# Kernel tuning notes

Measured on AMD Instinct MI355X. Metric: run time of the kernel, lower is better.

The kernel has to match this reference:

```python
import jax, jax.numpy as jnp
import numpy as np

B, D = 65536, 784          # batch, input features
H = 256                     # delegator feature (hidden) dim
L = 64                      # num_leaves (experts)
C = 10                      # num_classes


def setup_inputs() -> dict:
    key = jax.random.key(0)
    ks = jax.random.split(key, 7)
    s_in = 1.0 / np.sqrt(D)
    s_h = 1.0 / np.sqrt(H)
    return {
        "x": jax.random.normal(ks[0], (B, D), dtype=jnp.float32),
        "Wf": jax.random.normal(ks[1], (D, H), dtype=jnp.float32) * s_in,   # Node feature proj
        "bf": jnp.zeros((H,), dtype=jnp.float32),
        "Wr": jax.random.normal(ks[2], (D, L), dtype=jnp.float32) * s_in,   # Node router proj
        "br": jnp.zeros((L,), dtype=jnp.float32),
        "Wl": jax.random.normal(ks[3], (L, H, C), dtype=jnp.float32) * s_h,  # per-leaf linear
        "bl": jnp.zeros((L, C), dtype=jnp.float32),
    }


def reference(x, Wf, bf, Wr, br, Wl, bl):
    # Delegator (Node): features + routing probabilities
    features = jax.nn.relu(x @ Wf + bf)                 # [B, H]
    probs = jax.nn.softmax(x @ Wr + br, axis=1)         # [B, L]
    choices = jnp.argmax(probs, axis=1)                 # [B] top-1 leaf per sample
    # Per-sample leaf dispatch: gather each sample's leaf weights, then a
    # batched vec-mat product (memory-bound gather, low FLOP/byte).
    Wc = Wl[choices]                                    # [B, H, C]
    bc = bl[choices]                                    # [B, C]
    predictions = jnp.einsum("bh,bhc->bc", features, Wc) + bc  # [B, C]
    return predictions
```

## Files before the change

### kernel.cpp

```cpp
#include <hip/hip_runtime.h>
#include <stdint.h>

#define B_ROWS 65536
#define D_IN   784
#define H_DIM  256
#define L_LEAF 64
#define C_CLS  10
#define NSTEP2 25
#define BTILE2 20480
#define GAP_THRESH 0.03f

using f32x4    = __attribute__((ext_vector_type(4))) float;
using bf16x8   = __attribute__((ext_vector_type(8))) short;
using ushort8v = __attribute__((ext_vector_type(8))) unsigned short;
using ushort4v = __attribute__((ext_vector_type(4))) unsigned short;

#define O_FLAGCNT  0
#define O_CHOICES  4096
#define O_FLAGROWS (O_CHOICES + B_ROWS * 4)
#define O_WT       (O_FLAGROWS + B_ROWS * 4)
#define O_FEAT     (O_WT + NSTEP2 * BTILE2)
#define O_WLB      (O_FEAT + (size_t)B_ROWS * H_DIM * 2)
#define WLB_BYTES  ((size_t)L_LEAF * H_DIM * C_CLS * 2)
#define WS_BASE    O_WLB
#define WS_WLB     (O_WLB + WLB_BYTES)

__device__ __forceinline__ unsigned short f2bf(float f) {
    union { float f; unsigned int u; } c; c.f = f;
    unsigned int u = c.u;
    return (unsigned short)((u + 0x7fffu + ((u >> 16) & 1u)) >> 16);
}
__device__ __forceinline__ float bf2f(unsigned short u) {
    union { unsigned int u; float f; } c; c.u = ((unsigned int)u) << 16;
    return c.f;
}
__device__ __forceinline__ unsigned int cvtpk(float a, float b) {
    unsigned int r;
    asm("v_cvt_pk_bf16_f32 %0, %1, %2" : "=v"(r) : "v"(a), "v"(b));
    return r;
}
__device__ __forceinline__ void gload_lds16(const void* g, void* l) {
    __builtin_amdgcn_global_load_lds(
        (const __attribute__((address_space(1))) unsigned int*)g,
        (__attribute__((address_space(3))) unsigned int*)l, 16, 0, 0);
}

__global__ void k0_prep32(const float* __restrict__ Wf, const float* __restrict__ Wr,
                          unsigned short* __restrict__ Wt, unsigned int* __restrict__ flagcnt) {
    if (blockIdx.x == 0 && threadIdx.x == 0) *flagcnt = 0u;
    int id = blockIdx.x * 256 + threadIdx.x;
    int ts = id / 1280;
    int r  = id % 1280;
    int n  = r % 320;
    int c  = r / 320;
    int dst = ts * BTILE2 + ((n * 64 + c * 16) ^ ((n & 7) << 4));
    int ks  = ts * 32 + c * 8;
    unsigned short v[8];
    #pragma unroll
    for (int j = 0; j < 8; ++j) {
        int k = ks + j;
        float f = 0.f;
        if (k < D_IN)
            f = (n < H_DIM) ? Wf[(size_t)k * H_DIM + n]
                            : Wr[(size_t)k * L_LEAF + (n - H_DIM)];
        v[j] = f2bf(f);
    }
    *(ushort8v*)((char*)Wt + dst) = *(ushort8v*)v;
}

__global__ void k0b_wl(const float* __restrict__ Wl, unsigned short* __restrict__ Wlb) {
    int i = (blockIdx.x * 256 + threadIdx.x) * 4;
    f32x4 v = *(const f32x4*)(Wl + i);
    ushort4v h; h.x = f2bf(v.x); h.y = f2bf(v.y); h.z = f2bf(v.z); h.w = f2bf(v.w);
    *(ushort4v*)(Wlb + i) = h;
}

#define BUFB 36864
__global__ __launch_bounds__(512, 1) void k1_pipe(
    const float* __restrict__ x, const unsigned short* __restrict__ Wt,
    const float* __restrict__ bfv, const float* __restrict__ brv,
    unsigned short* __restrict__ feat, int* __restrict__ choices,
    unsigned int* __restrict__ flagcnt, int* __restrict__ flagrows)
{
    __shared__ __align__(16) char L[3 * BUFB];

    const int t  = threadIdx.x;
    const int w  = t >> 6, l = t & 63, q = l >> 4, ic = l & 15;
    const int wm = w >> 2, wn = w & 3;
    const int bm0 = blockIdx.x * 128;
    const int ntb = wn * 5;

    f32x4 acc[4][5];
    #pragma unroll
    for (int a = 0; a < 4; ++a)
        #pragma unroll
        for (int b = 0; b < 5; ++b)
            acc[a][b] = (f32x4){0.f, 0.f, 0.f, 0.f};

    const int e7  = ic & 7;
    const int pA0 = ((2 * q)     ^ e7) << 4;
    const int pA1 = ((2 * q + 1) ^ e7) << 4;
    const int rbB = (ic * 64 + (q << 4)) ^ (e7 << 4);

#define STAGE(TS, LB)                                                          \
    {                                                                          \
        const int ts_ = (TS);                                                  \
        char* Lb_ = (LB);                                                      \
        _Pragma("unroll")                                                      \
        for (int h = 0; h < 2; ++h) {                                          \
            int i_ = h * 512 + t;                                              \
            int r_ = i_ >> 3, p_ = i_ & 7;                                     \
            int c8_ = p_ ^ (r_ & 7);                                           \
            int k_ = ts_ * 32 + c8_ * 4;                                       \
            int ko_ = (k_ + 4 <= D_IN) ? k_ : 0;                               \
            gload_lds16(x + (size_t)(bm0 + r_) * D_IN + ko_, Lb_ + i_ * 16);   \
        }                                                                      \
        const char* bs_ = (const char*)Wt + (size_t)ts_ * BTILE2;              \
        char* bd_ = Lb_ + 16384;                                               \
        gload_lds16(bs_ + t * 16,          bd_ + t * 16);                      \
        gload_lds16(bs_ + (512 + t) * 16,  bd_ + (512 + t) * 16);              \
        if (t < 256)                                                           \
            gload_lds16(bs_ + (1024 + t) * 16, bd_ + (1024 + t) * 16);         \
    }

    STAGE(0, L);
    STAGE(1, L + BUFB);

    for (int ts = 0; ts < NSTEP2; ++ts) {
        if (ts < NSTEP2 - 1)
            asm volatile("s_waitcnt vmcnt(4)\ns_barrier" ::: "memory");
        else
            asm volatile("s_waitcnt vmcnt(0)\ns_barrier" ::: "memory");

        if (ts + 2 < NSTEP2) {
            char* nb = L + ((ts + 2) % 3) * BUFB;
            STAGE(ts + 2, nb);
        }

        const char* Lc = L + (ts % 3) * BUFB;
        bf16x8 af[4];
        #pragma unroll
        for (int mt = 0; mt < 4; ++mt) {
            const char* rowp = Lc + (wm * 64 + mt * 16 + ic) * 128;
            f32x4 lo = *(const f32x4*)(rowp + pA0);
            f32x4 hi = *(const f32x4*)(rowp + pA1);
            union { unsigned int u[4]; bf16x8 v; } pk;
            pk.u[0] = cvtpk(lo.x, lo.y);
            pk.u[1] = cvtpk(lo.z, lo.w);
            pk.u[2] = cvtpk(hi.x, hi.y);
            pk.u[3] = cvtpk(hi.z, hi.w);
            af[mt] = pk.v;
        }
        const char* Bb = Lc + 16384;
        __builtin_amdgcn_s_setprio(1);
        #pragma unroll
        for (int j = 0; j < 5; ++j) {
            bf16x8 b = *(const bf16x8*)(Bb + (ntb + j) * 1024 + rbB);
            #pragma unroll
            for (int mt = 0; mt < 4; ++mt)
                acc[mt][j] = __builtin_amdgcn_mfma_f32_16x16x32_bf16(af[mt], b, acc[mt][j], 0, 0, 0);
        }
        __builtin_amdgcn_s_setprio(0);
    }
#undef STAGE

    #pragma unroll
    for (int j = 0; j < 5; ++j) {
        int col = (ntb + j) * 16 + ic;
        if (col < H_DIM) {
            float bias = bfv[col];
            #pragma unroll
            for (int mt = 0; mt < 4; ++mt) {
                #pragma unroll
                for (int i = 0; i < 4; ++i) {
                    int row = bm0 + wm * 64 + mt * 16 + q * 4 + i;
                    float v = acc[mt][j][i] + bias;
                    v = v > 0.f ? v : 0.f;
                    feat[(size_t)row * H_DIM + col] = f2bf(v);
                }
            }
        }
    }
    if (wn == 3) {
        #pragma unroll
        for (int mt = 0; mt < 4; ++mt) {
            #pragma unroll
            for (int i = 0; i < 4; ++i) {
                float m1 = -1e30f, m2 = -1e30f;
                int a1 = 0;
                #pragma unroll
                for (int j = 1; j < 5; ++j) {
                    int leaf = (j - 1) * 16 + ic;
                    float v = acc[mt][j][i] + brv[leaf];
                    if (v > m1) { m2 = m1; m1 = v; a1 = leaf; }
                    else if (v > m2) { m2 = v; }
                }
                #pragma unroll
                for (int s = 1; s < 16; s <<= 1) {
                    float om1 = __shfl_xor(m1, s, 64);
                    float om2 = __shfl_xor(m2, s, 64);
                    int   oa1 = __shfl_xor(a1, s, 64);
                    bool take = (om1 > m1) || (om1 == m1 && oa1 < a1);
                    float nm2 = take ? fmaxf(om2, m1) : fmaxf(m2, om1);
                    m1 = take ? om1 : m1;
                    a1 = take ? oa1 : a1;
                    m2 = nm2;
                }
                if (ic == 0) {
                    int row = bm0 + wm * 64 + mt * 16 + q * 4 + i;
                    choices[row] = a1;
                    if (m1 - m2 < GAP_THRESH) {
                        unsigned int idx = atomicAdd(flagcnt, 1u);
                        flagrows[idx] = row;
                    }
                }
            }
        }
    }
}

__global__ __launch_bounds__(256) void k2_exact(
    const float* __restrict__ x, const float* __restrict__ Wr,
    const float* __restrict__ brv, const unsigned int* __restrict__ flagcnt,
    const int* __restrict__ flagrows, int* __restrict__ choices)
{
    __shared__ float wl[64 * 64];
    __shared__ float xl[4][64];
    const unsigned int cnt = *flagcnt;
    const int t = threadIdx.x, w = t >> 6, l = t & 63;
    for (unsigned int base = blockIdx.x * 4u; base < cnt; base += gridDim.x * 4u) {
        unsigned int ri = base + w;
        int row = (ri < cnt) ? flagrows[ri] : 0;
        const float* xr = x + (size_t)row * D_IN;
        float s0 = 0.f, s1 = 0.f, s2 = 0.f, s3 = 0.f;
        for (int kt = 0; kt < 13; ++kt) {
            int k0 = kt * 64;
            #pragma unroll
            for (int i = 0; i < 4; ++i) {
                int flat = i * 256 + t;
                int kk = flat >> 4, lq = (flat & 15) * 4;
                int kgk = k0 + kk;
                f32x4 v = (f32x4){0.f, 0.f, 0.f, 0.f};
                if (kgk < D_IN) v = *(const f32x4*)(Wr + (size_t)kgk * L_LEAF + lq);
                *(f32x4*)&wl[kk * 64 + lq] = v;
            }
            xl[w][l] = (k0 + l < D_IN) ? xr[k0 + l] : 0.f;
            __syncthreads();
            #pragma unroll
            for (int kk = 0; kk < 64; kk += 4) {
                s0 = fmaf(xl[w][kk    ], wl[(kk    ) * 64 + l], s0);
                s1 = fmaf(xl[w][kk + 1], wl[(kk + 1) * 64 + l], s1);
                s2 = fmaf(xl[w][kk + 2], wl[(kk + 2) * 64 + l], s2);
                s3 = fmaf(xl[w][kk + 3], wl[(kk + 3) * 64 + l], s3);
            }
            __syncthreads();
        }
        float v = (s0 + s1) + (s2 + s3) + brv[l];
        int a = l;
        #pragma unroll
        for (int st = 1; st < 64; st <<= 1) {
            float ov = __shfl_xor(v, st, 64);
            int   oa = __shfl_xor(a, st, 64);
            if (ov > v || (ov == v && oa < a)) { v = ov; a = oa; }
        }
        if (l == 0 && ri < cnt) choices[row] = a;
    }
}

__global__ __launch_bounds__(256) void k3_leaf(
    const unsigned short* __restrict__ feat, const int* __restrict__ choices,
    const float* __restrict__ Wl, const unsigned short* __restrict__ Wlb,
    const float* __restrict__ blv, float* __restrict__ out)
{
    const int t = threadIdx.x, wv = t >> 6, l = t & 63, g = l >> 4, i = l & 15;
    const int row = blockIdx.x * 16 + wv * 4 + g;
    const int leaf = choices[row];

    ushort8v f0 = *(const ushort8v*)(feat + (size_t)row * H_DIM + i * 16);
    ushort8v f1 = *(const ushort8v*)(feat + (size_t)row * H_DIM + i * 16 + 8);
    float fv[16];
    #pragma unroll
    for (int j = 0; j < 8; ++j) { fv[j] = bf2f(f0[j]); fv[8 + j] = bf2f(f1[j]); }

    float acc[C_CLS];
    #pragma unroll
    for (int c = 0; c < C_CLS; ++c) acc[c] = 0.f;

    if (Wlb) {
        const unsigned short* wp = Wlb + ((size_t)leaf * H_DIM + i * 16) * C_CLS;
        ushort8v wreg[20];
        #pragma unroll
        for (int j = 0; j < 20; ++j) wreg[j] = *(const ushort8v*)(wp + j * 8);
        #pragma unroll
        for (int h = 0; h < 16; ++h) {
            #pragma unroll
            for (int c = 0; c < C_CLS; ++c) {
                int e = h * C_CLS + c;
                acc[c] = fmaf(fv[h], bf2f(wreg[e >> 3][e & 7]), acc[c]);
            }
        }
    } else {
        const float* wp = Wl + ((size_t)leaf * H_DIM + i * 16) * C_CLS;
        #pragma unroll
        for (int h = 0; h < 16; ++h) {
            #pragma unroll
            for (int c = 0; c < C_CLS; ++c)
                acc[c] = fmaf(fv[h], wp[h * C_CLS + c], acc[c]);
        }
    }
    #pragma unroll
    for (int st = 1; st < 16; st <<= 1) {
        #pragma unroll
        for (int c = 0; c < C_CLS; ++c) acc[c] += __shfl_xor(acc[c], st, 64);
    }
    if (i == 0) {
        #pragma unroll
        for (int c = 0; c < C_CLS; ++c)
            out[(size_t)row * C_CLS + c] = acc[c] + blv[leaf * C_CLS + c];
    }
}

extern "C" void kernel_launch(void* const* d_in, const int* in_sizes, int n_in,
                              void* d_out, int out_size, void* d_ws, size_t ws_size,
                              hipStream_t stream) {
    if (ws_size < WS_BASE) return;
    const bool use_bf = ws_size >= WS_WLB;

    const float* x   = (const float*)d_in[0];
    const float* Wf  = (const float*)d_in[1];
    const float* bfv = (const float*)d_in[2];
    const float* Wr  = (const float*)d_in[3];
    const float* brv = (const float*)d_in[4];
    const float* Wl  = (const float*)d_in[5];
    const float* blv = (const float*)d_in[6];
    float* out = (float*)d_out;

    char* ws = (char*)d_ws;
    unsigned int*   flagcnt  = (unsigned int*)(ws + O_FLAGCNT);
    int*            choices  = (int*)(ws + O_CHOICES);
    int*            flagrows = (int*)(ws + O_FLAGROWS);
    unsigned short* Wt       = (unsigned short*)(ws + O_WT);
    unsigned short* feat     = (unsigned short*)(ws + O_FEAT);
    unsigned short* Wlb      = use_bf ? (unsigned short*)(ws + O_WLB) : (unsigned short*)0;

    hipLaunchKernelGGL(k0_prep32, dim3(125), dim3(256), 0, stream, Wf, Wr, Wt, flagcnt);
    if (use_bf)
        hipLaunchKernelGGL(k0b_wl, dim3(160), dim3(256), 0, stream, Wl, Wlb);
    hipLaunchKernelGGL(k1_pipe, dim3(B_ROWS / 128), dim3(512), 0, stream,
                       x, Wt, bfv, brv, feat, choices, flagcnt, flagrows);
    hipLaunchKernelGGL(k2_exact, dim3(1024), dim3(256), 0, stream,
                       x, Wr, brv, flagcnt, flagrows, choices);
    hipLaunchKernelGGL(k3_leaf, dim3(B_ROWS / 16), dim3(256), 0, stream,
                       feat, choices, Wl, Wlb, blv, out);
}
```

Before: 198.9 us.

## Enlarge fused GEMM block tile to 256 rows with 2x4 warp layout

The main feature/router GEMM kernel now processes 256 rows per block instead of 128. Its eight warps are rearranged as 4x2, so each warp computes 4x10 MFMA tiles instead of 4x5. This halves how many times the weight tile is loaded per row and gives more MFMA work per LDS B-fragment read. The cost is more accumulator registers, about 160 VGPRs for accumulators, and a larger LDS buffer. Only 256 blocks are launched, which may leave CUs underused. An explicit zero mask is added for the K tail.

```diff
diff --git a/kernel.cpp b/kernel.cpp
--- a/kernel.cpp
+++ b/kernel.cpp
@@ -75,8 +75,8 @@
     *(ushort4v*)(Wlb + i) = h;
 }
 
-#define BUFB 36864
-__global__ __launch_bounds__(512, 1) void k1_pipe(
+#define BUFB 53248
+__global__ __launch_bounds__(512, 1) void k1_big(
     const float* __restrict__ x, const unsigned short* __restrict__ Wt,
     const float* __restrict__ bfv, const float* __restrict__ brv,
     unsigned short* __restrict__ feat, int* __restrict__ choices,
@@ -86,15 +86,15 @@
 
     const int t  = threadIdx.x;
     const int w  = t >> 6, l = t & 63, q = l >> 4, ic = l & 15;
-    const int wm = w >> 2, wn = w & 3;
-    const int bm0 = blockIdx.x * 128;
-    const int ntb = wn * 5;
-
-    f32x4 acc[4][5];
+    const int wm = w >> 1, wn = w & 1;
+    const int bm0 = blockIdx.x * 256;
+    const int ntb = wn * 10;
+
+    f32x4 acc[4][10];
     #pragma unroll
     for (int a = 0; a < 4; ++a)
         #pragma unroll
-        for (int b = 0; b < 5; ++b)
+        for (int b = 0; b < 10; ++b)
             acc[a][b] = (f32x4){0.f, 0.f, 0.f, 0.f};
 
     const int e7  = ic & 7;
@@ -107,7 +107,7 @@
         const int ts_ = (TS);                                                  \
         char* Lb_ = (LB);                                                      \
         _Pragma("unroll")                                                      \
-        for (int h = 0; h < 2; ++h) {                                          \
+        for (int h = 0; h < 4; ++h) {                                          \
             int i_ = h * 512 + t;                                              \
             int r_ = i_ >> 3, p_ = i_ & 7;                                     \
             int c8_ = p_ ^ (r_ & 7);                                           \
@@ -116,7 +116,7 @@
             gload_lds16(x + (size_t)(bm0 + r_) * D_IN + ko_, Lb_ + i_ * 16);   \
         }                                                                      \
         const char* bs_ = (const char*)Wt + (size_t)ts_ * BTILE2;              \
-        char* bd_ = Lb_ + 16384;                                               \
+        char* bd_ = Lb_ + 32768;                                               \
         gload_lds16(bs_ + t * 16,          bd_ + t * 16);                      \
         gload_lds16(bs_ + (512 + t) * 16,  bd_ + (512 + t) * 16);              \
         if (t < 256)                                                           \
@@ -128,7 +128,7 @@
 
     for (int ts = 0; ts < NSTEP2; ++ts) {
         if (ts < NSTEP2 - 1)
-            asm volatile("s_waitcnt vmcnt(4)\ns_barrier" ::: "memory");
+            asm volatile("s_waitcnt vmcnt(6)\ns_barrier" ::: "memory");
         else
             asm volatile("s_waitcnt vmcnt(0)\ns_barrier" ::: "memory");
 
@@ -138,6 +138,8 @@
         }
 
         const char* Lc = L + (ts % 3) * BUFB;
+        const int kg = ts * 32 + q * 8;
+        const bool ok = (kg + 8 <= D_IN);
         bf16x8 af[4];
         #pragma unroll
         for (int mt = 0; mt < 4; ++mt) {
@@ -145,28 +147,28 @@
             f32x4 lo = *(const f32x4*)(rowp + pA0);
             f32x4 hi = *(const f32x4*)(rowp + pA1);
             union { unsigned int u[4]; bf16x8 v; } pk;
-            pk.u[0] = cvtpk(lo.x, lo.y);
-            pk.u[1] = cvtpk(lo.z, lo.w);
-            pk.u[2] = cvtpk(hi.x, hi.y);
-            pk.u[3] = cvtpk(hi.z, hi.w);
+            pk.u[0] = ok ? cvtpk(lo.x, lo.y) : 0u;
+            pk.u[1] = ok ? cvtpk(lo.z, lo.w) : 0u;
+            pk.u[2] = ok ? cvtpk(hi.x, hi.y) : 0u;
+            pk.u[3] = ok ? cvtpk(hi.z, hi.w) : 0u;
             af[mt] = pk.v;
         }
-        const char* Bb = Lc + 16384;
+        const char* Bb = Lc + 32768;
         __builtin_amdgcn_s_setprio(1);
         #pragma unroll
-        for (int j = 0; j < 5; ++j) {
-            bf16x8 b = *(const bf16x8*)(Bb + (ntb + j) * 1024 + rbB);
+        for (int nt = 0; nt < 10; ++nt) {
+            bf16x8 b = *(const bf16x8*)(Bb + (ntb + nt) * 1024 + rbB);
             #pragma unroll
             for (int mt = 0; mt < 4; ++mt)
-                acc[mt][j] = __builtin_amdgcn_mfma_f32_16x16x32_bf16(af[mt], b, acc[mt][j], 0, 0, 0);
+                acc[mt][nt] = __builtin_amdgcn_mfma_f32_16x16x32_bf16(af[mt], b, acc[mt][nt], 0, 0, 0);
         }
         __builtin_amdgcn_s_setprio(0);
     }
 #undef STAGE
 
     #pragma unroll
-    for (int j = 0; j < 5; ++j) {
-        int col = (ntb + j) * 16 + ic;
+    for (int nt = 0; nt < 10; ++nt) {
+        int col = (ntb + nt) * 16 + ic;
         if (col < H_DIM) {
             float bias = bfv[col];
             #pragma unroll
@@ -174,14 +176,14 @@
                 #pragma unroll
                 for (int i = 0; i < 4; ++i) {
                     int row = bm0 + wm * 64 + mt * 16 + q * 4 + i;
-                    float v = acc[mt][j][i] + bias;
+                    float v = acc[mt][nt][i] + bias;
                     v = v > 0.f ? v : 0.f;
                     feat[(size_t)row * H_DIM + col] = f2bf(v);
                 }
             }
         }
     }
-    if (wn == 3) {
+    if (wn == 1) {
         #pragma unroll
         for (int mt = 0; mt < 4; ++mt) {
             #pragma unroll
@@ -189,9 +191,9 @@
                 float m1 = -1e30f, m2 = -1e30f;
                 int a1 = 0;
                 #pragma unroll
-                for (int j = 1; j < 5; ++j) {
-                    int leaf = (j - 1) * 16 + ic;
-                    float v = acc[mt][j][i] + brv[leaf];
+                for (int nt = 6; nt < 10; ++nt) {
+                    int leaf = (nt - 6) * 16 + ic;
+                    float v = acc[mt][nt][i] + brv[leaf];
                     if (v > m1) { m2 = m1; m1 = v; a1 = leaf; }
                     else if (v > m2) { m2 = v; }
                 }
@@ -346,7 +348,7 @@
     hipLaunchKernelGGL(k0_prep32, dim3(125), dim3(256), 0, stream, Wf, Wr, Wt, flagcnt);
     if (use_bf)
         hipLaunchKernelGGL(k0b_wl, dim3(160), dim3(256), 0, stream, Wl, Wlb);
-    hipLaunchKernelGGL(k1_pipe, dim3(B_ROWS / 128), dim3(512), 0, stream,
+    hipLaunchKernelGGL(k1_big, dim3(B_ROWS / 256), dim3(512), 0, stream,
                        x, Wt, bfv, brv, feat, choices, flagcnt, flagrows);
     hipLaunchKernelGGL(k2_exact, dim3(1024), dim3(256), 0, stream,
                        x, Wr, brv, flagcnt, flagrows, choices);
```

Result: no change. 197.3 us (-0.8%).
